# Performance work log

Measured on AMD Instinct MI355X. Metric: run time of the kernel, lower is better.

The kernel has to match this reference:

```python
import jax, jax.numpy as jnp
import numpy as np

B, L, D, H, K = 8, 2048, 1024, 4, 4
HD = D // H  # head_dim = 256
EPS_NORM = 1e-12  # F.normalize clamp
RMS_EPS = 1e-05


def setup_inputs() -> dict:
    key = jax.random.key(0)
    ks = jax.random.split(key, 10)
    s = 0.02
    return {
        "x": jax.random.normal(ks[0], (B, L, D), dtype=jnp.float32),
        "Wq": jax.random.normal(ks[1], (D, D), dtype=jnp.float32) * s,
        "Wk": jax.random.normal(ks[2], (D, D), dtype=jnp.float32) * s,
        "Wv": jax.random.normal(ks[3], (D, D), dtype=jnp.float32) * s,
        "cq": jax.random.normal(ks[4], (D, 1, K), dtype=jnp.float32) * 0.2,
        "ck": jax.random.normal(ks[5], (D, 1, K), dtype=jnp.float32) * 0.2,
        "cv": jax.random.normal(ks[6], (D, 1, K), dtype=jnp.float32) * 0.2,
        "Wbeta": jax.random.normal(ks[7], (H, D), dtype=jnp.float32) * s,
        "rms_w": jnp.ones((D,), dtype=jnp.float32),
        "Wout": jax.random.normal(ks[8], (D, D), dtype=jnp.float32) * s,
    }


def _causal_dwconv_silu(y, w):
    # y: [B, L, D], w: [D, 1, K] (torch Conv1d depthwise weight, cross-correlation)
    yt = jnp.transpose(y, (0, 2, 1))  # [B, D, L]
    out = jax.lax.conv_general_dilated(
        yt, w, window_strides=(1,), padding=[(K - 1, 0)],
        dimension_numbers=("NCH", "OIH", "NCH"), feature_group_count=D)
    return jnp.transpose(jax.nn.silu(out), (0, 2, 1))  # [B, L, D]


def _l2norm(x):
    n = jnp.sqrt(jnp.sum(x * x, axis=-1, keepdims=True))
    return x / jnp.maximum(n, EPS_NORM)


def reference(x, Wq, Wk, Wv, cq, ck, cv, Wbeta, rms_w, Wout):
    q = x @ Wq.T
    k = x @ Wk.T
    v = x @ Wv.T
    # depthwise causal conv + silu, then reshape to heads, then silu again (as in source)
    q = jax.nn.silu(_causal_dwconv_silu(q, cq).reshape(B, L, H, HD))
    k = jax.nn.silu(_causal_dwconv_silu(k, ck).reshape(B, L, H, HD))
    v = jax.nn.silu(_causal_dwconv_silu(v, cv).reshape(B, L, H, HD))
    q = _l2norm(q)
    k = _l2norm(k)
    beta = jax.nn.sigmoid(x @ Wbeta.T)  # [B, L, H]

    # time-major for scan: [L, B, H, d]
    kT = jnp.transpose(k, (1, 0, 2, 3))
    qT = jnp.transpose(q, (1, 0, 2, 3))
    vT = jnp.transpose(v, (1, 0, 2, 3))
    bT = jnp.transpose(beta, (1, 0, 2))  # [L, B, H]

    S0 = jnp.zeros((B, H, HD, HD), dtype=x.dtype)

    def step(S, inp):
        k_t, q_t, v_t, b_t = inp
        Sk = jnp.einsum("bhij,bhj->bhi", S, k_t)
        upd = (Sk - v_t)[..., :, None] * k_t[..., None, :]  # outer product [B,H,d,d]
        S = S - b_t[..., None, None] * upd
        o = jnp.einsum("bhij,bhj->bhi", S, q_t)
        return S, o

    S_final, o_all = jax.lax.scan(step, S0, (kT, qT, vT, bT))
    o = o_all[-1].reshape(B, D)  # only last timestep's output is used

    # RMSNorm + output projection
    o = o * jax.lax.rsqrt(jnp.mean(o * o, axis=-1, keepdims=True) + RMS_EPS) * rms_w
    o = o @ Wout.T
    return o, S_final
```

## Files before the change

kernel.cpp:

```cpp
#include <hip/hip_runtime.h>

#define LL 2048
#define BB 8
#define DD 1024
#define HH 4
#define HD 256

#define AS1 __attribute__((address_space(1)))
#define AS3 __attribute__((address_space(3)))

typedef __attribute__((ext_vector_type(8))) short short8;
typedef __attribute__((ext_vector_type(4))) float f32x4;
typedef unsigned short u16;
typedef unsigned int u32;

static __device__ __forceinline__ u16 f2bf(float f) {
    u32 u = __float_as_uint(f);
    return (u16)((u + 0x7fffu + ((u >> 16) & 1u)) >> 16);
}
static __device__ __forceinline__ float bf2f(u16 v) {
    return __uint_as_float(((u32)v) << 16);
}
static __device__ __forceinline__ float silu2_fast(float x) {
    float s1 = x * __builtin_amdgcn_rcpf(1.0f + __expf(-x));
    return s1 * __builtin_amdgcn_rcpf(1.0f + __expf(-s1));
}

#define BAR_LGKM() do { \
    asm volatile("s_waitcnt lgkmcnt(0)" ::: "memory"); \
    __builtin_amdgcn_s_barrier(); \
    __builtin_amdgcn_sched_barrier(0); \
} while (0)

static __device__ __forceinline__ void cvt8_plain(const float* __restrict__ in,
                                                  u16* __restrict__ out, int blk, int n) {
    int i = (blk * 256 + (int)threadIdx.x) * 8;
    if (i >= n) return;
    float4 a = *(const float4*)(in + i);
    float4 b = *(const float4*)(in + i + 4);
    uint4 pk;
    pk.x = (u32)f2bf(a.x) | ((u32)f2bf(a.y) << 16);
    pk.y = (u32)f2bf(a.z) | ((u32)f2bf(a.w) << 16);
    pk.z = (u32)f2bf(b.x) | ((u32)f2bf(b.y) << 16);
    pk.w = (u32)f2bf(b.z) | ((u32)f2bf(b.w) << 16);
    *(uint4*)(out + i) = pk;
}

__global__ __launch_bounds__(256) void front_kernel(
    const float* __restrict__ x, const float* __restrict__ Wk, const float* __restrict__ Wv,
    const float* __restrict__ Wbeta, const float* __restrict__ Wq,
    u16* __restrict__ XB, u16* __restrict__ WKVB, float* __restrict__ BETA,
    u16* __restrict__ RQ)
{
    __shared__ float wsum[4][4];
    const int blk = blockIdx.x;
    const int tid = threadIdx.x;
    if (blk < 8192) {
        const long base = (long)blk * 2048 + tid * 8;
        float4 a = *(const float4*)(x + base);
        float4 b = *(const float4*)(x + base + 4);
        uint4 pk;
        pk.x = (u32)f2bf(a.x) | ((u32)f2bf(a.y) << 16);
        pk.y = (u32)f2bf(a.z) | ((u32)f2bf(a.w) << 16);
        pk.z = (u32)f2bf(b.x) | ((u32)f2bf(b.y) << 16);
        pk.w = (u32)f2bf(b.z) | ((u32)f2bf(b.w) << 16);
        *(uint4*)(XB + base) = pk;

        const int col = (tid * 8) & 1023;
        float s[4];
#pragma unroll
        for (int h = 0; h < 4; h++) {
            const float* wr = Wbeta + (long)h * DD + col;
            float4 w0 = *(const float4*)wr;
            float4 w1 = *(const float4*)(wr + 4);
            s[h] = a.x * w0.x + a.y * w0.y + a.z * w0.z + a.w * w0.w +
                   b.x * w1.x + b.y * w1.y + b.z * w1.z + b.w * w1.w;
        }
#pragma unroll
        for (int h = 0; h < 4; h++)
#pragma unroll
            for (int m = 1; m < 64; m <<= 1) s[h] += __shfl_xor(s[h], m);
        const int w = tid >> 6, lane = tid & 63;
        if (lane == 0) {
#pragma unroll
            for (int h = 0; h < 4; h++) wsum[w][h] = s[h];
        }
        __syncthreads();
        if (tid < 8) {
            int r = tid >> 2, h = tid & 3;
            float v = wsum[2 * r][h] + wsum[2 * r + 1][h];
            BETA[((long)blk * 2 + r) * HH + h] = 1.0f / (1.0f + __expf(-v));
        }
    } else if (blk < 8704) {
        cvt8_plain(Wk, WKVB, blk - 8192, 1048576);
    } else if (blk < 9216) {
        cvt8_plain(Wv, WKVB + 1048576, blk - 8704, 1048576);
    } else {
        const int w = tid >> 6, lane = tid & 63;
        const int n = (blk - 9216) * 4 + w;
        const float* wr = Wq + (long)n * DD + lane * 16;
        float4 wv_[4];
#pragma unroll
        for (int u = 0; u < 4; u++) wv_[u] = *(const float4*)(wr + u * 4);
#pragma unroll 4
        for (int m = 0; m < 32; m++) {
            const int bb = m >> 2, j = m & 3;
            const float* xr = x + ((long)bb * LL + (LL - 4 + j)) * DD + lane * 16;
            float s = 0.f;
#pragma unroll
            for (int u = 0; u < 4; u++) {
                float4 av = *(const float4*)(xr + u * 4);
                s += av.x * wv_[u].x + av.y * wv_[u].y + av.z * wv_[u].z + av.w * wv_[u].w;
            }
#pragma unroll
            for (int mm = 1; mm < 64; mm <<= 1) s += __shfl_xor(s, mm);
            if (lane == 0) RQ[(long)m * DD + n] = f2bf(s);
        }
    }
}

__global__ __launch_bounds__(512, 1) void gemm_8ph(const u16* __restrict__ A,
                                                   const u16* __restrict__ W,
                                                   u16* __restrict__ C) {
    __shared__ __align__(16) char sm_[131072];
    const int tid = threadIdx.x;
    const int w = tid >> 6, lane = tid & 63, g = lane >> 4, c = lane & 15;
    const int wm_ = w >> 2, wn_ = w & 3;
    const int bid = blockIdx.x;
    const int by = (bid & 7) * 8 + ((bid >> 3) >> 3);
    const int bx = (bid >> 3) & 7;
    const int m0 = by * 256, n0 = bx * 256;
    const int sr = tid >> 3, cb = (tid & 7) * 16;
    const int ssw = (sr & 7) << 4;
    const int sw = (c & 7) << 4;

    f32x4 acc[8][4];
#pragma unroll
    for (int i = 0; i < 8; i++)
#pragma unroll
        for (int j = 0; j < 4; j++) acc[i][j] = (f32x4){0.f, 0.f, 0.f, 0.f};
    short8 afr[4][2];
    short8 bfr[2][2];

#define GL8(gp, lofs) __builtin_amdgcn_global_load_lds((const AS1 void*)(gp), \
        (AS3 void*)((AS3 char*)sm_ + (lofs)), 16, 0, 0)
#define ST_A(kt, half, PB) { \
    const char* gp_ = (const char*)A + ((long)(m0 + (half)*128 + sr) * 1024 + (kt) * 64) * 2 + (cb ^ ssw); \
    GL8(gp_, (PB) + (half)*16384 + tid*16); GL8(gp_ + 131072, (PB) + (half)*16384 + 8192 + tid*16); }
#define ST_B(kt, half, PB) { \
    const char* gp_ = (const char*)W + ((long)(n0 + (half)*128 + sr) * 1024 + (kt) * 64) * 2 + (cb ^ ssw); \
    GL8(gp_, 65536 + (PB) + (half)*16384 + tid*16); GL8(gp_ + 131072, 65536 + (PB) + (half)*16384 + 8192 + tid*16); }
#define LOADA(qm, PB) { \
    const char* ab_ = sm_ + (PB) + wm_ * 16384 + ((qm) * 64 + c) * 128; \
    _Pragma("unroll") for (int mt = 0; mt < 4; mt++) \
        _Pragma("unroll") for (int ks = 0; ks < 2; ks++) \
            afr[mt][ks] = *(const short8*)(ab_ + mt * 2048 + ((ks * 64 + g * 16) ^ sw)); }
#define LOADB(qn, PB) { \
    const char* bb_ = sm_ + 65536 + (PB) + (wn_ >> 1) * 16384 + ((wn_ & 1) * 64 + (qn) * 32 + c) * 128; \
    _Pragma("unroll") for (int nt = 0; nt < 2; nt++) \
        _Pragma("unroll") for (int ks = 0; ks < 2; ks++) \
            bfr[nt][ks] = *(const short8*)(bb_ + nt * 2048 + ((ks * 64 + g * 16) ^ sw)); }
#define MFMAQ(qm, qn) { \
    __builtin_amdgcn_s_barrier(); \
    __builtin_amdgcn_s_setprio(1); \
    _Pragma("unroll") for (int mt = 0; mt < 4; mt++) \
        _Pragma("unroll") for (int nt = 0; nt < 2; nt++) \
            _Pragma("unroll") for (int ks = 0; ks < 2; ks++) \
                acc[(qm)*4+mt][(qn)*2+nt] = __builtin_amdgcn_mfma_f32_16x16x32_bf16( \
                    afr[mt][ks], bfr[nt][ks], acc[(qm)*4+mt][(qn)*2+nt], 0, 0, 0); \
    __builtin_amdgcn_s_setprio(0); }
#define ENDB() { __builtin_amdgcn_s_barrier(); __builtin_amdgcn_sched_barrier(0); }

    ST_A(0, 0, 0) ST_A(0, 1, 0) ST_B(0, 0, 0) ST_B(0, 1, 0) ST_A(1, 0, 32768)
    asm volatile("s_waitcnt vmcnt(2)" ::: "memory");
    __builtin_amdgcn_s_barrier();
    __builtin_amdgcn_sched_barrier(0);

    for (int u = 0; u < 8; ++u) {
        const int t1k = 2 * u + 1, nk = 2 * u + 2, nk1 = 2 * u + 3;
        const bool more = (u < 7);
        LOADA(0, 0) LOADB(0, 0) ST_A(t1k, 1, 32768) MFMAQ(0, 0) ENDB()
        LOADB(1, 0) ST_B(t1k, 0, 32768) MFMAQ(0, 1) ENDB()
        LOADA(1, 0) LOADB(0, 0) ST_B(t1k, 1, 32768) MFMAQ(1, 0) ENDB()
        LOADB(1, 0)
        if (more) ST_A(nk, 0, 0)
        MFMAQ(1, 1)
        if (more) { asm volatile("s_waitcnt vmcnt(2)" ::: "memory"); }
        else      { asm volatile("s_waitcnt vmcnt(0)" ::: "memory"); }
        ENDB()
        LOADA(0, 32768) LOADB(0, 32768)
        if (more) ST_B(nk, 0, 0)
        MFMAQ(0, 0) ENDB()
        LOADB(1, 32768)
        if (more) ST_A(nk, 1, 0)
        MFMAQ(0, 1) ENDB()
        LOADA(1, 32768) LOADB(0, 32768)
        if (more) ST_B(nk, 1, 0)
        MFMAQ(1, 0) ENDB()
        LOADB(1, 32768)
        if (more) ST_A(nk1, 0, 32768)
        MFMAQ(1, 1)
        if (more) { asm volatile("s_waitcnt vmcnt(2)" ::: "memory"); }
        ENDB()
    }

#pragma unroll
    for (int mt = 0; mt < 8; mt++)
#pragma unroll
        for (int nt = 0; nt < 4; nt++)
#pragma unroll
            for (int r = 0; r < 4; r++)
                C[(long)(m0 + wm_ * 128 + mt * 16 + 4 * g + r) * 2048 +
                  n0 + wn_ * 64 + nt * 16 + c] = f2bf(acc[mt][nt][r]);
#undef GL8
#undef ST_A
#undef ST_B
#undef LOADA
#undef LOADB
#undef MFMAQ
#undef ENDB
}

__global__ __launch_bounds__(256, 3) void prep_fused(
    const u16* __restrict__ R, const float* __restrict__ ck, const float* __restrict__ cv,
    const float* __restrict__ cq, const u16* __restrict__ RQ, const float* __restrict__ BETA,
    u16* __restrict__ LK_g, u16* __restrict__ BKT_g, u16* __restrict__ LV_g,
    u16* __restrict__ QN)
{
    __shared__ __align__(16) char pm[50688];
    const int blk = blockIdx.x;
    const int tid = threadIdx.x;

    if (blk >= 1024) {
        const int b = blk - 1024;
        const int d = tid * 4;
        float w0[4], w1[4], w2[4], w3[4];
        const float4* cw4 = (const float4*)cq;
        *(float4*)w0 = cw4[d + 0];
        *(float4*)w1 = cw4[d + 1];
        *(float4*)w2 = cw4[d + 2];
        *(float4*)w3 = cw4[d + 3];
        const u16* base = RQ + (long)b * 4 * DD + d;
        float a0 = 0.f, a1 = 0.f, a2 = 0.f, a3 = 0.f;
#pragma unroll
        for (int j = 0; j < 4; j++) {
            uint2 v = *(const uint2*)(base + (long)j * DD);
            a0 += bf2f((u16)(v.x & 0xffff)) * w0[j];
            a1 += bf2f((u16)(v.x >> 16)) * w1[j];
            a2 += bf2f((u16)(v.y & 0xffff)) * w2[j];
            a3 += bf2f((u16)(v.y >> 16)) * w3[j];
        }
        float y0 = silu2_fast(a0);
        float y1 = silu2_fast(a1);
        float y2 = silu2_fast(a2);
        float y3 = silu2_fast(a3);
        float ss = y0 * y0 + y1 * y1 + y2 * y2 + y3 * y3;
#pragma unroll
        for (int m = 1; m < 64; m <<= 1) ss += __shfl_xor(ss, m);
        float sc = 1.0f / fmaxf(sqrtf(ss), 1e-12f);
        y0 *= sc; y1 *= sc; y2 *= sc; y3 *= sc;
        uint2 o;
        o.x = (u32)f2bf(y0) | ((u32)f2bf(y1) << 16);
        o.y = (u32)f2bf(y2) | ((u32)f2bf(y3) << 16);
        *(uint2*)(QN + ((long)b * 4 + 3) * DD + d) = o;
        return;
    }

    const int bh = blk >> 5, q = blk & 31;
    const int b = bh >> 2, h = bh & 3;
    const int w = tid >> 6, lane = tid & 63, g = lane >> 4, c = lane & 15;
    const long cb = (long)(bh * 32 + q);
    u16* WLp = (u16*)(pm + 32768);
    float* bv   = (float*)(pm + 49664);
    float* n2   = (float*)(pm + 49920);
    float* invn = (float*)(pm + 50176);
    float* ncl  = (float*)(pm + 50432);

    if (tid < 64) bv[tid] = BETA[((long)b * LL + 64 * q + tid) * HH + h];

    f32x4 aacc[4];
#pragma unroll
    for (int nt = 0; nt < 4; nt++) aacc[nt] = (f32x4){0.f, 0.f, 0.f, 0.f};

    const int dloc = tid & 127, th = tid >> 7;
#pragma unroll
    for (int pass = 0; pass < 2; pass++) {
        {
            const int dg = pass * 128 + dloc;
            float4 wt = ((const float4*)ck)[h * HD + dg];
            const u16* rp = R + ((long)b * LL + 64 * q) * 2048 + h * HD + dg;
            u16 arr[35];
            if (q == 0 && th == 0) {
                arr[0] = 0; arr[1] = 0; arr[2] = 0;
#pragma unroll
                for (int i = 3; i < 35; i++) arr[i] = rp[(long)(i - 3) * 2048];
            } else {
                const u16* rb = rp + (long)(32 * th - 3) * 2048;
#pragma unroll
                for (int i = 0; i < 35; i++) arr[i] = rb[(long)i * 2048];
            }
            u16 vals[8];
#pragma unroll
            for (int jj = 0; jj < 32; jj++) {
                int t = 32 * th + jj;
                float y = bf2f(arr[jj]) * wt.x + bf2f(arr[jj + 1]) * wt.y +
                          bf2f(arr[jj + 2]) * wt.z + bf2f(arr[jj + 3]) * wt.w;
                y = silu2_fast(y);
                u16 yb = f2bf(y);
                vals[t & 7] = yb;
                *(u16*)(pm + 32768 + t * 256 + ((((dloc >> 3) ^ (t & 7)) << 4) + (dloc & 7) * 2)) = yb;
                if ((t & 7) == 7)
                    *(uint4*)(pm + dg * 128 + (((t >> 3) ^ (dg & 7)) << 4)) = *(uint4*)vals;
            }
        }
        BAR_LGKM();
        {
            const int ra = 16 * w + c;
#pragma unroll
            for (int q8 = 0; q8 < 4; q8++) {
                short8 af = *(const short8*)(pm + 32768 + ra * 256 + (((4 * q8 + g) ^ (ra & 7)) << 4));
#pragma unroll
                for (int nt = 0; nt < 4; nt++) {
                    const int rb = 16 * nt + c;
                    short8 bf = *(const short8*)(pm + 32768 + rb * 256 + (((4 * q8 + g) ^ (rb & 7)) << 4));
                    aacc[nt] = __builtin_amdgcn_mfma_f32_16x16x32_bf16(af, bf, aacc[nt], 0, 0, 0);
                }
            }
        }
        BAR_LGKM();
    }

#pragma unroll
    for (int nt = 0; nt < 4; nt++)
        if (nt == w && (c >> 2) == g) n2[16 * w + c] = aacc[nt][c & 3];
    BAR_LGKM();
    if (tid < 64) {
        float nn = fmaxf(sqrtf(n2[tid]), 1e-12f);
        ncl[tid] = nn;
        invn[tid] = 1.0f / nn;
    }
    BAR_LGKM();

    {
#pragma unroll
        for (int nt = 0; nt < 4; nt++)
#pragma unroll
            for (int r = 0; r < 4; r++) {
                int tt = 16 * w + 4 * g + r, s = 16 * nt + c;
                WLp[tt * 68 + s] = f2bf(aacc[nt][r] * bv[s] * invn[tt] * invn[s]);
            }
        for (int ii = tid; ii < 2048; ii += 256) {
            int dd = ii >> 3, bl = ii & 7;
            u16 vals[8];
            *(uint4*)vals = *(const uint4*)(pm + dd * 128 + bl * 16);
            int t0 = (bl ^ (dd & 7)) << 3;
#pragma unroll
            for (int j = 0; j < 8; j++)
                vals[j] = f2bf(bf2f(vals[j]) * bv[t0 + j] * invn[t0 + j]);
            *(uint4*)((char*)(BKT_g + cb * 16384) + dd * 128 + bl * 16) = *(uint4*)vals;
        }
    }
    BAR_LGKM();

    {
        const int col = 16 * w + c;
        const float sc_col = invn[col];
        float li[16];
#pragma unroll
        for (int u = 0; u < 16; u++) li[u] = (4 * u + g == col) ? 1.0f : 0.0f;
#pragma unroll
        for (int t = 1; t < 64; t++) {
            float acc = 0.f;
#pragma unroll
            for (int u = 0; u <= (t - 1) / 4; u++) {
                int s = 4 * u + g;
                if (s < t) acc += bf2f(WLp[t * 68 + s]) * li[u];
            }
            acc += __shfl_xor(acc, 16);
            acc += __shfl_xor(acc, 32);
            float val = ((t == col) ? 1.0f : 0.0f) - acc;
            if ((t & 3) == g) li[t >> 2] = val;
        }
#pragma unroll
        for (int u = 0; u < 16; u++) {
            int s = 4 * u + g;
            *(u16*)(pm + 41472 + s * 128 + ((((col >> 3) ^ (s & 7)) << 4) + (col & 7) * 2)) =
                f2bf(li[u] * sc_col);
        }
    }
    BAR_LGKM();

    {
        f32x4 lk[4][4];
#pragma unroll
        for (int i = 0; i < 4; i++)
#pragma unroll
            for (int j = 0; j < 4; j++) lk[i][j] = (f32x4){0.f, 0.f, 0.f, 0.f};
#pragma unroll
        for (int qs = 0; qs < 2; qs++) {
            short8 aL[4], bK[4];
#pragma unroll
            for (int mt = 0; mt < 4; mt++)
                aL[mt] = *(const short8*)(pm + 41472 + (16 * mt + c) * 128 +
                                          (((qs * 4 + g) ^ (c & 7)) << 4));
#pragma unroll
            for (int dn = 0; dn < 4; dn++)
                bK[dn] = *(const short8*)(pm + (64 * w + 16 * dn + c) * 128 +
                                          (((qs * 4 + g) ^ (c & 7)) << 4));
#pragma unroll
            for (int mt = 0; mt < 4; mt++)
#pragma unroll
                for (int dn = 0; dn < 4; dn++)
                    lk[mt][dn] = __builtin_amdgcn_mfma_f32_16x16x32_bf16(aL[mt], bK[dn], lk[mt][dn], 0, 0, 0);
        }
        char* lkg = (char*)(LK_g + cb * 16384);
#pragma unroll
        for (int mt = 0; mt < 4; mt++)
#pragma unroll
            for (int dn = 0; dn < 4; dn++)
#pragma unroll
                for (int r = 0; r < 4; r++) {
                    int t = 16 * mt + 4 * g + r;
                    int d = 64 * w + 16 * dn + c;
                    *(u16*)(lkg + t * 512 + ((((d >> 3) ^ (t & 7)) << 4) + (d & 7) * 2)) =
                        f2bf(-lk[mt][dn][r]);
                }
    }
    BAR_LGKM();

    {
        float4 wt = ((const float4*)cv)[h * HD + tid];
        const u16* rp = R + ((long)b * LL + 64 * q) * 2048 + 1024 + h * HD + tid;
#pragma unroll
        for (int hh = 0; hh < 2; hh++) {
            u16 arr[35];
            if (q == 0 && hh == 0) {
                arr[0] = 0; arr[1] = 0; arr[2] = 0;
#pragma unroll
                for (int i = 3; i < 35; i++) arr[i] = rp[(long)(i - 3) * 2048];
            } else {
                const u16* rb = rp + (long)(32 * hh - 3) * 2048;
#pragma unroll
                for (int i = 0; i < 35; i++) arr[i] = rb[(long)i * 2048];
            }
            u16 vals[8];
#pragma unroll
            for (int jj = 0; jj < 32; jj++) {
                int t = 32 * hh + jj;
                float y = bf2f(arr[jj]) * wt.x + bf2f(arr[jj + 1]) * wt.y +
                          bf2f(arr[jj + 2]) * wt.z + bf2f(arr[jj + 3]) * wt.w;
                y = silu2_fast(y) * ncl[t];
                vals[t & 7] = f2bf(y);
                if ((t & 7) == 7)
                    *(uint4*)(pm + tid * 128 + (((t >> 3) ^ (tid & 7)) << 4)) = *(uint4*)vals;
            }
        }
    }
    BAR_LGKM();

    {
        f32x4 lv[4][4];
#pragma unroll
        for (int i = 0; i < 4; i++)
#pragma unroll
            for (int j = 0; j < 4; j++) lv[i][j] = (f32x4){0.f, 0.f, 0.f, 0.f};
#pragma unroll
        for (int qs = 0; qs < 2; qs++) {
            short8 aL[4], bV[4];
#pragma unroll
            for (int mt = 0; mt < 4; mt++)
                aL[mt] = *(const short8*)(pm + 41472 + (16 * mt + c) * 128 +
                                          (((qs * 4 + g) ^ (c & 7)) << 4));
#pragma unroll
            for (int dn = 0; dn < 4; dn++)
                bV[dn] = *(const short8*)(pm + (64 * w + 16 * dn + c) * 128 +
                                          (((qs * 4 + g) ^ (c & 7)) << 4));
#pragma unroll
            for (int mt = 0; mt < 4; mt++)
#pragma unroll
                for (int dn = 0; dn < 4; dn++)
                    lv[mt][dn] = __builtin_amdgcn_mfma_f32_16x16x32_bf16(aL[mt], bV[dn], lv[mt][dn], 0, 0, 0);
        }
        u32* lvg = (u32*)LV_g + cb * 8192;
#pragma unroll
        for (int mt = 0; mt < 4; mt++)
#pragma unroll
            for (int dn = 0; dn < 4; dn++) {
                int iblk = 2 * w + (dn >> 1);
                int it = dn & 1;
                int base = iblk * 1024 + 64 * (2 * mt + it) + 16 * g + c;
                lvg[base]       = (u32)f2bf(lv[mt][dn][0]) | ((u32)f2bf(lv[mt][dn][1]) << 16);
                lvg[base + 512] = (u32)f2bf(lv[mt][dn][2]) | ((u32)f2bf(lv[mt][dn][3]) << 16);
            }
    }
}

__global__ __launch_bounds__(512, 1) void scan_chunked(
    const u16* __restrict__ LK_g, const u16* __restrict__ BKT_g,
    const u16* __restrict__ LV_g, const u16* __restrict__ QN,
    float* __restrict__ out, float* __restrict__ ORAW)
{
    __shared__ __align__(16) char smem[159744];
    const int blk = blockIdx.x;
    const int bh = blk & 31, iblk = blk >> 5;
    const int b = bh >> 2, h = bh & 3;
    const int row0 = iblk * 32;
    const int tid = threadIdx.x;
    const int w = tid >> 6, lane = tid & 63, g = lane >> 4, c = lane & 15;
    const int mt = w >> 1, it = w & 1;
    const int sw = (c & 7) << 4;

#define GLDS16(gp, lofs) __builtin_amdgcn_global_load_lds((const AS1 void*)(gp), \
        (AS3 void*)((AS3 char*)smem + (lofs)), 16, 0, 0)
#define GLDS4(gp, lofs) __builtin_amdgcn_global_load_lds((const AS1 void*)(gp), \
        (AS3 void*)((AS3 char*)smem + (lofs)), 4, 0, 0)
#define STAGE_LK(qq, bi) { const char* gp = (const char*)(LK_g + (long)(bh * 32 + (qq)) * 16384); \
    _Pragma("unroll") for (int i_ = 0; i_ < 4; i_++) GLDS16(gp + i_ * 8192 + tid * 16, (bi) * 32768 + i_ * 8192 + tid * 16); }
#define STAGE_BKT(qq, bi) { const char* gp = (const char*)(BKT_g + (long)(bh * 32 + (qq)) * 16384); \
    _Pragma("unroll") for (int i_ = 0; i_ < 4; i_++) GLDS16(gp + i_ * 8192 + tid * 16, 65536 + (bi) * 32768 + i_ * 8192 + tid * 16); }
#define STAGE_LV(qq, bi) { const char* gp = (const char*)LV_g + (long)(bh * 32 + (qq)) * 32768 + iblk * 4096; \
    GLDS4(gp + tid * 4, 131072 + (bi) * 4096 + tid * 4); \
    GLDS4(gp + 2048 + tid * 4, 131072 + (bi) * 4096 + 2048 + tid * 4); }

    f32x4 S[2][2];
#pragma unroll
    for (int si = 0; si < 2; si++)
#pragma unroll
        for (int sj = 0; sj < 2; sj++) S[si][sj] = (f32x4){0.f, 0.f, 0.f, 0.f};

    STAGE_LK(0, 0); STAGE_BKT(0, 0); STAGE_LV(0, 0);

    for (int q = 0; q < 32; ++q) {
        const int cur = q & 1;
        if (q < 31) {
            STAGE_LK(q + 1, cur ^ 1); STAGE_BKT(q + 1, cur ^ 1); STAGE_LV(q + 1, cur ^ 1);
            asm volatile("s_waitcnt vmcnt(10)" ::: "memory");
        } else {
            asm volatile("s_waitcnt vmcnt(0)" ::: "memory");
        }
        __builtin_amdgcn_s_barrier();
        __builtin_amdgcn_sched_barrier(0);

        const char* lkb = smem + cur * 32768;
        const char* bkb = smem + 65536 + cur * 32768;
        const char* lvb = smem + 131072 + cur * 4096;

        u32 l0 = *(const u32*)(lvb + tid * 4);
        u32 l1 = *(const u32*)(lvb + 2048 + tid * 4);
        f32x4 w0, w1;
        w0[0] = bf2f((u16)(l0 & 0xffff)); w0[1] = bf2f((u16)(l0 >> 16));
        w0[2] = bf2f((u16)(l1 & 0xffff)); w0[3] = bf2f((u16)(l1 >> 16));
        w1 = (f32x4){0.f, 0.f, 0.f, 0.f};
        if (q > 0) {
            const int arow = (16 * mt + c) * 512;
            const int brow = (16 * it + c) * 512;
            __builtin_amdgcn_s_setprio(1);
#pragma unroll
            for (int q8 = 0; q8 < 8; q8++) {
                short8 av = *(const short8*)(lkb + arow + (((q8 * 4 + g) << 4) ^ sw));
                short8 bv8 = *(const short8*)(smem + 143360 + brow + (((q8 * 4 + g) << 4) ^ sw));
                if (q8 & 1) w1 = __builtin_amdgcn_mfma_f32_16x16x32_bf16(av, bv8, w1, 0, 0, 0);
                else        w0 = __builtin_amdgcn_mfma_f32_16x16x32_bf16(av, bv8, w0, 0, 0, 0);
            }
            __builtin_amdgcn_s_setprio(0);
#pragma unroll
            for (int r = 0; r < 4; r++) w0[r] += w1[r];
        }

        {
            char* ub = smem + 139264 + (16 * it + c) * 128;
#pragma unroll
            for (int r = 0; r < 4; r++) {
                int t = 16 * mt + 4 * g + r;
                *(u16*)(ub + ((((t >> 3) << 4) ^ sw) + (t & 7) * 2)) = f2bf(w0[r]);
            }
        }
        asm volatile("s_waitcnt lgkmcnt(0)" ::: "memory");
        __builtin_amdgcn_s_barrier();
        __builtin_amdgcn_sched_barrier(0);

        __builtin_amdgcn_s_setprio(1);
#pragma unroll
        for (int Qp = 0; Qp < 2; Qp++) {
            const int tof = ((Qp * 4 + g) << 4) ^ sw;
            short8 a0 = *(const short8*)(smem + 139264 + c * 128 + tof);
            short8 a1 = *(const short8*)(smem + 139264 + (16 + c) * 128 + tof);
            short8 b0 = *(const short8*)(bkb + (32 * w + c) * 128 + tof);
            short8 b1 = *(const short8*)(bkb + (32 * w + 16 + c) * 128 + tof);
            S[0][0] = __builtin_amdgcn_mfma_f32_16x16x32_bf16(a0, b0, S[0][0], 0, 0, 0);
            S[0][1] = __builtin_amdgcn_mfma_f32_16x16x32_bf16(a0, b1, S[0][1], 0, 0, 0);
            S[1][0] = __builtin_amdgcn_mfma_f32_16x16x32_bf16(a1, b0, S[1][0], 0, 0, 0);
            S[1][1] = __builtin_amdgcn_mfma_f32_16x16x32_bf16(a1, b1, S[1][1], 0, 0, 0);
        }
        __builtin_amdgcn_s_setprio(0);

        if (q < 31) {
#pragma unroll
            for (int si = 0; si < 2; si++)
#pragma unroll
                for (int sj = 0; sj < 2; sj++)
#pragma unroll
                    for (int r = 0; r < 4; r++) {
                        int i = 16 * si + 4 * g + r;
                        *(u16*)(smem + 143360 + i * 512 +
                                ((((4 * w + 2 * sj + (c >> 3)) << 4) ^ ((i & 7) << 4)) + (c & 7) * 2)) =
                            f2bf(S[si][sj][r]);
                    }
        }
        asm volatile("s_waitcnt lgkmcnt(0)" ::: "memory");
        __builtin_amdgcn_s_barrier();
        __builtin_amdgcn_sched_barrier(0);
    }

    float op[2][4];
#pragma unroll
    for (int si = 0; si < 2; si++)
#pragma unroll
        for (int r = 0; r < 4; r++) op[si][r] = 0.f;
#pragma unroll
    for (int sj = 0; sj < 2; sj++) {
        const float qv = bf2f(QN[((long)b * 4 + 3) * DD + h * HD + 32 * w + 16 * sj + c]);
#pragma unroll
        for (int si = 0; si < 2; si++)
#pragma unroll
            for (int r = 0; r < 4; r++) op[si][r] += S[si][sj][r] * qv;
    }
#pragma unroll
    for (int si = 0; si < 2; si++)
#pragma unroll
        for (int r = 0; r < 4; r++) {
            float v = op[si][r];
            v += __shfl_xor(v, 1); v += __shfl_xor(v, 2);
            v += __shfl_xor(v, 4); v += __shfl_xor(v, 8);
            op[si][r] = v;
        }
    float* red = (float*)smem;
    if (c == 0) {
#pragma unroll
        for (int si = 0; si < 2; si++)
#pragma unroll
            for (int r = 0; r < 4; r++) red[w * 32 + 16 * si + 4 * g + r] = op[si][r];
    }
    __syncthreads();
    if (tid < 32) {
        float o = 0.f;
#pragma unroll
        for (int ww = 0; ww < 8; ww++) o += red[ww * 32 + tid];
        ORAW[(long)b * DD + h * HD + row0 + tid] = o;
    }
#pragma unroll
    for (int si = 0; si < 2; si++)
#pragma unroll
        for (int sj = 0; sj < 2; sj++)
#pragma unroll
            for (int r = 0; r < 4; r++)
                out[8192 + ((long)(bh * 256 + row0 + 16 * si + 4 * g + r)) * 256
                    + 32 * w + 16 * sj + c] = S[si][sj][r];
#undef GLDS16
#undef GLDS4
#undef STAGE_LK
#undef STAGE_BKT
#undef STAGE_LV
}

__global__ __launch_bounds__(256) void tail_kernel(const float* __restrict__ ORAW,
                                                   const float* __restrict__ rms_w,
                                                   const float* __restrict__ Wout,
                                                   float* __restrict__ out) {
    const int b = blockIdx.x >> 8;
    const int n = (blockIdx.x & 255) * 4 + (threadIdx.x >> 6);
    const int lane = threadIdx.x & 63;
    const int t = threadIdx.x;

    float4 v = *(const float4*)(ORAW + (long)b * DD + t * 4);
    float ss = v.x * v.x + v.y * v.y + v.z * v.z + v.w * v.w;
#pragma unroll
    for (int m = 1; m < 64; m <<= 1) ss += __shfl_xor(ss, m);
    __shared__ float wsum[4];
    if ((t & 63) == 0) wsum[t >> 6] = ss;
    __syncthreads();
    float tot = wsum[0] + wsum[1] + wsum[2] + wsum[3];
    float sc = rsqrtf(tot / (float)DD + 1e-5f);

    const float* orow = ORAW + (long)b * DD + lane * 16;
    const float* grow = rms_w + lane * 16;
    const float* wrow = Wout + (long)n * DD + lane * 16;
    float s = 0.f;
#pragma unroll
    for (int u = 0; u < 4; u++) {
        float4 a = *(const float4*)(orow + u * 4);
        float4 gw = *(const float4*)(grow + u * 4);
        float4 ww = *(const float4*)(wrow + u * 4);
        s += a.x * sc * gw.x * ww.x + a.y * sc * gw.y * ww.y +
             a.z * sc * gw.z * ww.z + a.w * sc * gw.w * ww.w;
    }
#pragma unroll
    for (int m = 1; m < 64; m <<= 1) s += __shfl_xor(s, m);
    if (lane == 0) out[(long)b * DD + n] = s;
}

extern "C" void kernel_launch(void* const* d_in, const int* in_sizes, int n_in,
                              void* d_out, int out_size, void* d_ws, size_t ws_size,
                              hipStream_t stream) {
    const float* x     = (const float*)d_in[0];
    const float* Wq    = (const float*)d_in[1];
    const float* Wk    = (const float*)d_in[2];
    const float* Wv    = (const float*)d_in[3];
    const float* cq    = (const float*)d_in[4];
    const float* ck    = (const float*)d_in[5];
    const float* cv    = (const float*)d_in[6];
    const float* Wbeta = (const float*)d_in[7];
    const float* rms_w = (const float*)d_in[8];
    const float* Wout  = (const float*)d_in[9];
    float* out = (float*)d_out;

    char* ws = (char*)d_ws;
    u16* XB     = (u16*)(ws + 0);
    u16* BKT_g  = (u16*)(ws + 0);
    u16* WKVB   = (u16*)(ws + 33554432);
    u16* R      = (u16*)(ws + 37748736);
    u16* LK_g   = (u16*)(ws + 104857600);
    u16* LV_g   = (u16*)(ws + 138412032);
    float* BETA = (float*)(ws + 171966464);
    u16* RQ     = (u16*)(ws + 172228608);
    u16* QN     = (u16*)(ws + 172294144);
    float* ORAW = (float*)(ws + 172359680);

    front_kernel<<<9472, 256, 0, stream>>>(x, Wk, Wv, Wbeta, Wq, XB, WKVB, BETA, RQ);
    gemm_8ph<<<512, 512, 0, stream>>>(XB, WKVB, R);
    prep_fused<<<1032, 256, 0, stream>>>(R, ck, cv, cq, RQ, BETA, LK_g, BKT_g, LV_g, QN);
    scan_chunked<<<256, 512, 0, stream>>>(LK_g, BKT_g, LV_g, QN, out, ORAW);
    tail_kernel<<<2048, 256, 0, stream>>>(ORAW, rms_w, Wout, out);
}
```

Before: 237.7 us.

## Load LK operand directly into registers with double-buffered prefetch instead of LDS

The scan loop stops staging the per-chunk LK matrix through shared memory and instead has each wave load its own MFMA A-fragments straight from global memory into two alternating register arrays, prefetched one chunk ahead. The loop is unrolled by two so the register buffers can swap without copies, and the LDS footprint shrinks from about 156KB to 92KB. This removes LDS write/read traffic and bank pressure for LK but adds register pressure, and the end-of-step wait now drains all outstanding global loads, which can expose load latency.

```diff
diff --git a/kernel.cpp b/kernel.cpp
--- a/kernel.cpp
+++ b/kernel.cpp
@@ -500,7 +500,7 @@
     const u16* __restrict__ LV_g, const u16* __restrict__ QN,
     float* __restrict__ out, float* __restrict__ ORAW)
 {
-    __shared__ __align__(16) char smem[159744];
+    __shared__ __align__(16) char smem[94208];
     const int blk = blockIdx.x;
     const int bh = blk & 31, iblk = blk >> 5;
     const int b = bh >> 2, h = bh & 3;
@@ -514,13 +514,15 @@
         (AS3 void*)((AS3 char*)smem + (lofs)), 16, 0, 0)
 #define GLDS4(gp, lofs) __builtin_amdgcn_global_load_lds((const AS1 void*)(gp), \
         (AS3 void*)((AS3 char*)smem + (lofs)), 4, 0, 0)
-#define STAGE_LK(qq, bi) { const char* gp = (const char*)(LK_g + (long)(bh * 32 + (qq)) * 16384); \
+#define STAGE_BKT(qq, bi) { const char* gp = (const char*)(BKT_g + (long)(bh * 32 + (qq)) * 16384); \
     _Pragma("unroll") for (int i_ = 0; i_ < 4; i_++) GLDS16(gp + i_ * 8192 + tid * 16, (bi) * 32768 + i_ * 8192 + tid * 16); }
-#define STAGE_BKT(qq, bi) { const char* gp = (const char*)(BKT_g + (long)(bh * 32 + (qq)) * 16384); \
-    _Pragma("unroll") for (int i_ = 0; i_ < 4; i_++) GLDS16(gp + i_ * 8192 + tid * 16, 65536 + (bi) * 32768 + i_ * 8192 + tid * 16); }
 #define STAGE_LV(qq, bi) { const char* gp = (const char*)LV_g + (long)(bh * 32 + (qq)) * 32768 + iblk * 4096; \
-    GLDS4(gp + tid * 4, 131072 + (bi) * 4096 + tid * 4); \
-    GLDS4(gp + 2048 + tid * 4, 131072 + (bi) * 4096 + 2048 + tid * 4); }
+    GLDS4(gp + tid * 4, 65536 + (bi) * 4096 + tid * 4); \
+    GLDS4(gp + 2048 + tid * 4, 65536 + (bi) * 4096 + 2048 + tid * 4); }
+#define LKLOAD(dst, qq) { \
+    const char* base_ = (const char*)LK_g + (long)(bh * 32 + (qq)) * 32768 + (16 * mt + c) * 512; \
+    _Pragma("unroll") for (int q8 = 0; q8 < 8; q8++) \
+        dst[q8] = *(const short8*)(base_ + (((q8 * 4 + g) << 4) ^ sw)); }
 
     f32x4 S[2][2];
 #pragma unroll
@@ -528,88 +530,86 @@
 #pragma unroll
         for (int sj = 0; sj < 2; sj++) S[si][sj] = (f32x4){0.f, 0.f, 0.f, 0.f};
 
-    STAGE_LK(0, 0); STAGE_BKT(0, 0); STAGE_LV(0, 0);
-
-    for (int q = 0; q < 32; ++q) {
-        const int cur = q & 1;
-        if (q < 31) {
-            STAGE_LK(q + 1, cur ^ 1); STAGE_BKT(q + 1, cur ^ 1); STAGE_LV(q + 1, cur ^ 1);
-            asm volatile("s_waitcnt vmcnt(10)" ::: "memory");
-        } else {
-            asm volatile("s_waitcnt vmcnt(0)" ::: "memory");
-        }
-        __builtin_amdgcn_s_barrier();
-        __builtin_amdgcn_sched_barrier(0);
-
-        const char* lkb = smem + cur * 32768;
-        const char* bkb = smem + 65536 + cur * 32768;
-        const char* lvb = smem + 131072 + cur * 4096;
-
-        u32 l0 = *(const u32*)(lvb + tid * 4);
-        u32 l1 = *(const u32*)(lvb + 2048 + tid * 4);
-        f32x4 w0, w1;
-        w0[0] = bf2f((u16)(l0 & 0xffff)); w0[1] = bf2f((u16)(l0 >> 16));
-        w0[2] = bf2f((u16)(l1 & 0xffff)); w0[3] = bf2f((u16)(l1 >> 16));
-        w1 = (f32x4){0.f, 0.f, 0.f, 0.f};
-        if (q > 0) {
-            const int arow = (16 * mt + c) * 512;
-            const int brow = (16 * it + c) * 512;
-            __builtin_amdgcn_s_setprio(1);
-#pragma unroll
-            for (int q8 = 0; q8 < 8; q8++) {
-                short8 av = *(const short8*)(lkb + arow + (((q8 * 4 + g) << 4) ^ sw));
-                short8 bv8 = *(const short8*)(smem + 143360 + brow + (((q8 * 4 + g) << 4) ^ sw));
-                if (q8 & 1) w1 = __builtin_amdgcn_mfma_f32_16x16x32_bf16(av, bv8, w1, 0, 0, 0);
-                else        w0 = __builtin_amdgcn_mfma_f32_16x16x32_bf16(av, bv8, w0, 0, 0, 0);
-            }
-            __builtin_amdgcn_s_setprio(0);
-#pragma unroll
-            for (int r = 0; r < 4; r++) w0[r] += w1[r];
-        }
-
-        {
-            char* ub = smem + 139264 + (16 * it + c) * 128;
-#pragma unroll
-            for (int r = 0; r < 4; r++) {
-                int t = 16 * mt + 4 * g + r;
-                *(u16*)(ub + ((((t >> 3) << 4) ^ sw) + (t & 7) * 2)) = f2bf(w0[r]);
-            }
-        }
-        asm volatile("s_waitcnt lgkmcnt(0)" ::: "memory");
-        __builtin_amdgcn_s_barrier();
-        __builtin_amdgcn_sched_barrier(0);
-
-        __builtin_amdgcn_s_setprio(1);
-#pragma unroll
-        for (int Qp = 0; Qp < 2; Qp++) {
-            const int tof = ((Qp * 4 + g) << 4) ^ sw;
-            short8 a0 = *(const short8*)(smem + 139264 + c * 128 + tof);
-            short8 a1 = *(const short8*)(smem + 139264 + (16 + c) * 128 + tof);
-            short8 b0 = *(const short8*)(bkb + (32 * w + c) * 128 + tof);
-            short8 b1 = *(const short8*)(bkb + (32 * w + 16 + c) * 128 + tof);
-            S[0][0] = __builtin_amdgcn_mfma_f32_16x16x32_bf16(a0, b0, S[0][0], 0, 0, 0);
-            S[0][1] = __builtin_amdgcn_mfma_f32_16x16x32_bf16(a0, b1, S[0][1], 0, 0, 0);
-            S[1][0] = __builtin_amdgcn_mfma_f32_16x16x32_bf16(a1, b0, S[1][0], 0, 0, 0);
-            S[1][1] = __builtin_amdgcn_mfma_f32_16x16x32_bf16(a1, b1, S[1][1], 0, 0, 0);
-        }
-        __builtin_amdgcn_s_setprio(0);
-
-        if (q < 31) {
-#pragma unroll
-            for (int si = 0; si < 2; si++)
-#pragma unroll
-                for (int sj = 0; sj < 2; sj++)
-#pragma unroll
-                    for (int r = 0; r < 4; r++) {
-                        int i = 16 * si + 4 * g + r;
-                        *(u16*)(smem + 143360 + i * 512 +
-                                ((((4 * w + 2 * sj + (c >> 3)) << 4) ^ ((i & 7) << 4)) + (c & 7) * 2)) =
-                            f2bf(S[si][sj][r]);
-                    }
-        }
-        asm volatile("s_waitcnt lgkmcnt(0)" ::: "memory");
-        __builtin_amdgcn_s_barrier();
-        __builtin_amdgcn_sched_barrier(0);
+    short8 lkA[8], lkB[8];
+
+    LKLOAD(lkA, 0)
+    STAGE_BKT(0, 0); STAGE_LV(0, 0);
+    asm volatile("s_waitcnt vmcnt(0)" ::: "memory");
+    __builtin_amdgcn_s_barrier();
+    __builtin_amdgcn_sched_barrier(0);
+
+#define BODY(q, LKC, LKN)                                                                 \
+    {                                                                                     \
+        const int cur = (q) & 1;                                                          \
+        if ((q) < 31) { LKLOAD(LKN, (q) + 1) STAGE_BKT((q) + 1, cur ^ 1); STAGE_LV((q) + 1, cur ^ 1); } \
+        const char* bkb = smem + cur * 32768;                                             \
+        const char* lvb = smem + 65536 + cur * 4096;                                      \
+        u32 l0 = *(const u32*)(lvb + tid * 4);                                            \
+        u32 l1 = *(const u32*)(lvb + 2048 + tid * 4);                                     \
+        f32x4 w0, w1;                                                                     \
+        w0[0] = bf2f((u16)(l0 & 0xffff)); w0[1] = bf2f((u16)(l0 >> 16));                  \
+        w0[2] = bf2f((u16)(l1 & 0xffff)); w0[3] = bf2f((u16)(l1 >> 16));                  \
+        w1 = (f32x4){0.f, 0.f, 0.f, 0.f};                                                 \
+        if ((q) > 0) {                                                                    \
+            const int brow = (16 * it + c) * 512;                                         \
+            __builtin_amdgcn_s_setprio(1);                                                \
+            _Pragma("unroll")                                                             \
+            for (int q8 = 0; q8 < 8; q8++) {                                              \
+                short8 bv8 = *(const short8*)(smem + 77824 + brow + (((q8 * 4 + g) << 4) ^ sw)); \
+                if (q8 & 1) w1 = __builtin_amdgcn_mfma_f32_16x16x32_bf16(LKC[q8], bv8, w1, 0, 0, 0); \
+                else        w0 = __builtin_amdgcn_mfma_f32_16x16x32_bf16(LKC[q8], bv8, w0, 0, 0, 0); \
+            }                                                                             \
+            __builtin_amdgcn_s_setprio(0);                                                \
+            _Pragma("unroll")                                                             \
+            for (int r = 0; r < 4; r++) w0[r] += w1[r];                                   \
+        }                                                                                 \
+        {                                                                                 \
+            char* ub = smem + 73728 + (16 * it + c) * 128;                                \
+            _Pragma("unroll")                                                             \
+            for (int r = 0; r < 4; r++) {                                                 \
+                int t = 16 * mt + 4 * g + r;                                              \
+                *(u16*)(ub + ((((t >> 3) << 4) ^ sw) + (t & 7) * 2)) = f2bf(w0[r]);       \
+            }                                                                             \
+        }                                                                                 \
+        asm volatile("s_waitcnt lgkmcnt(0)" ::: "memory");                                \
+        __builtin_amdgcn_s_barrier();                                                     \
+        __builtin_amdgcn_sched_barrier(0);                                                \
+        __builtin_amdgcn_s_setprio(1);                                                    \
+        _Pragma("unroll")                                                                 \
+        for (int Qp = 0; Qp < 2; Qp++) {                                                  \
+            const int tof = ((Qp * 4 + g) << 4) ^ sw;                                     \
+            short8 a0 = *(const short8*)(smem + 73728 + c * 128 + tof);                   \
+            short8 a1 = *(const short8*)(smem + 73728 + (16 + c) * 128 + tof);            \
+            short8 b0 = *(const short8*)(bkb + (32 * w + c) * 128 + tof);                 \
+            short8 b1 = *(const short8*)(bkb + (32 * w + 16 + c) * 128 + tof);            \
+            S[0][0] = __builtin_amdgcn_mfma_f32_16x16x32_bf16(a0, b0, S[0][0], 0, 0, 0);  \
+            S[0][1] = __builtin_amdgcn_mfma_f32_16x16x32_bf16(a0, b1, S[0][1], 0, 0, 0);  \
+            S[1][0] = __builtin_amdgcn_mfma_f32_16x16x32_bf16(a1, b0, S[1][0], 0, 0, 0);  \
+            S[1][1] = __builtin_amdgcn_mfma_f32_16x16x32_bf16(a1, b1, S[1][1], 0, 0, 0);  \
+        }                                                                                 \
+        __builtin_amdgcn_s_setprio(0);                                                    \
+        if ((q) < 31) {                                                                   \
+            _Pragma("unroll")                                                             \
+            for (int si = 0; si < 2; si++)                                                \
+                _Pragma("unroll")                                                         \
+                for (int sj = 0; sj < 2; sj++)                                            \
+                    _Pragma("unroll")                                                     \
+                    for (int r = 0; r < 4; r++) {                                         \
+                        int i = 16 * si + 4 * g + r;                                      \
+                        *(u16*)(smem + 77824 + i * 512 +                                  \
+                                ((((4 * w + 2 * sj + (c >> 3)) << 4) ^ ((i & 7) << 4)) + (c & 7) * 2)) = \
+                            f2bf(S[si][sj][r]);                                           \
+                    }                                                                     \
+        }                                                                                 \
+        asm volatile("s_waitcnt vmcnt(0) lgkmcnt(0)" ::: "memory");                       \
+        __builtin_amdgcn_s_barrier();                                                     \
+        __builtin_amdgcn_sched_barrier(0);                                                \
+    }
+
+#pragma unroll 1
+    for (int qq = 0; qq < 16; ++qq) {
+        BODY(2 * qq, lkA, lkB)
+        BODY(2 * qq + 1, lkB, lkA)
     }
 
     float op[2][4];
@@ -658,9 +658,10 @@
                     + 32 * w + 16 * sj + c] = S[si][sj][r];
 #undef GLDS16
 #undef GLDS4
-#undef STAGE_LK
 #undef STAGE_BKT
 #undef STAGE_LV
+#undef LKLOAD
+#undef BODY
 }
 
 __global__ __launch_bounds__(256) void tail_kernel(const float* __restrict__ ORAW,
```

Result: slower. 243.0 us (+2.2%).
